# Kernel optimization log

Measured on AMD Instinct MI355X. Metric: run time of the kernel, lower is better.

## Reference

```python
import jax, jax.numpy as jnp
import numpy as np

UNITS = [100, 80, 50, 30]
D_IN = 64


def _lstm_layer(x, Wx, Wh, b):
    # x: [B, T, D]; Wx: [D, 4u]; Wh: [u, 4u]; b: [4u]
    B = x.shape[0]
    u = Wh.shape[0]
    # precompute input contribution for all timesteps: [B, T, 4u]
    xg = jnp.einsum('btd,dg->btg', x, Wx) + b

    def step(carry, xg_t):
        h, c = carry
        g = xg_t + h @ Wh                      # [B, 4u]
        i, f, cbar, o = jnp.split(g, 4, axis=-1)
        i = jax.nn.sigmoid(i)
        f = jax.nn.sigmoid(f)
        o = jax.nn.sigmoid(o)
        c = f * c + i * jnp.tanh(cbar)
        h = o * jnp.tanh(c)
        return (h, c), h

    init = (jnp.zeros((B, u), x.dtype), jnp.zeros((B, u), x.dtype))
    (h_final, _), hs = jax.lax.scan(step, init, jnp.swapaxes(xg, 0, 1))
    return jnp.swapaxes(hs, 0, 1), h_final  # [B, T, u], [B, u]


def setup_inputs() -> dict:
    key = jax.random.key(0)
    ks = jax.random.split(key, 16)
    B, T = 256, 1024
    inp = {"sequence": jax.random.normal(ks[0], (B, T, D_IN), dtype=jnp.float32)}
    d_in = D_IN
    for li, u in enumerate(UNITS):
        s_x = 1.0 / np.sqrt(d_in)
        s_h = 1.0 / np.sqrt(u)
        inp[f"Wx{li}"] = jax.random.normal(ks[1 + 3 * li], (d_in, 4 * u), dtype=jnp.float32) * s_x
        inp[f"Wh{li}"] = jax.random.normal(ks[2 + 3 * li], (u, 4 * u), dtype=jnp.float32) * s_h
        inp[f"b{li}"] = jnp.zeros((4 * u,), dtype=jnp.float32)
        d_in = u
    inp["W_out"] = jax.random.normal(ks[13], (UNITS[-1], 1), dtype=jnp.float32) / np.sqrt(UNITS[-1])
    inp["b_out"] = jnp.zeros((1,), dtype=jnp.float32)
    return inp


def reference(sequence, Wx0, Wh0, b0, Wx1, Wh1, b1, Wx2, Wh2, b2, Wx3, Wh3, b3, W_out, b_out):
    # 4 stacked LSTM layers; dropout is identity at inference.
    x, _ = _lstm_layer(sequence, Wx0, Wh0, b0)   # [B, T, 100]
    x, _ = _lstm_layer(x, Wx1, Wh1, b1)          # [B, T, 80]
    x, _ = _lstm_layer(x, Wx2, Wh2, b2)          # [B, T, 50]
    _, h = _lstm_layer(x, Wx3, Wh3, b3)          # final state [B, 30]
    return h @ W_out + b_out                     # [B, 1]
```

## Files before the change

### kernel.cpp

```cpp
#include <hip/hip_runtime.h>


#define BATCH 256
#define TFULL 1024
#define TC    128
#define NCHUNK (TFULL / TC)

__device__ __forceinline__ float fast_rcp(float x) {
    return __builtin_amdgcn_rcpf(x);
}

__device__ __forceinline__ float tanh_fast(float x) {
    float e = __expf(-2.0f * fabsf(x));
    float r = fast_rcp(1.0f + e);
    return copysignf(fmaf(2.0f, r, -1.0f), x);
}

__device__ __forceinline__ void lds_barrier() {
    asm volatile("s_waitcnt lgkmcnt(0)\n\ts_barrier" ::: "memory");
}

template<int CTRL>
__device__ __forceinline__ float dpp_add(float v) {
    int t = __builtin_amdgcn_update_dpp(0, __float_as_int(v), CTRL, 0xF, 0xF, true);
    return v + __int_as_float(t);
}
template<int CTRL>
__device__ __forceinline__ float dpp_mov(float v) {
    int t = __builtin_amdgcn_update_dpp(0, __float_as_int(v), CTRL, 0xF, 0xF, true);
    return __int_as_float(t);
}

template<int K, int N>
__global__ __launch_bounds__(256, 2)
void xg_gemm(const float* __restrict__ x, int batchStride,
             const float* __restrict__ Wx,
             const float* __restrict__ bias,
             float* __restrict__ out)
{
    constexpr int K4   = (K + 3) / 4;
    constexpr int SLAB = 64 * 4 + 4;

    const int n0   = blockIdx.x * 64;
    const int row0 = blockIdx.y * 64;
    const int tid  = threadIdx.x;
    const int tx   = tid & 15;
    const int ty   = tid >> 4;

    __shared__ __align__(16) float s_A[K4 * SLAB];
    __shared__ __align__(16) float s_B[K4 * 4 * 64];

    if constexpr ((K % 4) == 0) {
        for (int i = tid; i < 64 * (K / 4); i += 256) {
            const int row = i / (K / 4);
            const int k4  = i % (K / 4);
            const int gr  = row0 + row;
            const int b   = gr >> 7;
            const int t   = gr & 127;
            float4 v = *(const float4*)(x + (size_t)b * batchStride + t * K + k4 * 4);
            *(float4*)(s_A + k4 * SLAB + row * 4) = v;
        }
    } else {
        for (int i = tid; i < 64 * K; i += 256) {
            const int row = i / K;
            const int k   = i % K;
            const int gr  = row0 + row;
            const int b   = gr >> 7;
            const int t   = gr & 127;
            s_A[(k >> 2) * SLAB + row * 4 + (k & 3)] =
                x[(size_t)b * batchStride + t * K + k];
        }
        constexpr int PAD = K4 * 4 - K;
        for (int i = tid; i < 64 * PAD; i += 256) {
            const int row = i / PAD;
            const int kk  = K + i % PAD;
            s_A[(kk >> 2) * SLAB + row * 4 + (kk & 3)] = 0.0f;
        }
    }

    for (int i = tid; i < K4 * 4 * 16; i += 256) {
        const int k  = i >> 4;
        const int c4 = i & 15;
        float4 v = {0.0f, 0.0f, 0.0f, 0.0f};
        if (k < K && n0 + c4 * 4 < N)
            v = *(const float4*)(Wx + (size_t)k * N + n0 + c4 * 4);
        *(float4*)(s_B + k * 64 + c4 * 4) = v;
    }
    __syncthreads();

    float acc[4][4];
#pragma unroll
    for (int r = 0; r < 4; ++r)
#pragma unroll
        for (int c = 0; c < 4; ++c) acc[r][c] = 0.0f;

    for (int k4 = 0; k4 < K4; ++k4) {
        float4 bv[4];
#pragma unroll
        for (int j = 0; j < 4; ++j)
            bv[j] = *(const float4*)(s_B + (k4 * 4 + j) * 64 + tx * 4);
#pragma unroll
        for (int r = 0; r < 4; ++r) {
            float4 av = *(const float4*)(s_A + k4 * SLAB + (ty + 16 * r) * 4);
#pragma unroll
            for (int c = 0; c < 4; ++c) {
                acc[r][c] = fmaf(av.x, ((const float*)&bv[0])[c], acc[r][c]);
                acc[r][c] = fmaf(av.y, ((const float*)&bv[1])[c], acc[r][c]);
                acc[r][c] = fmaf(av.z, ((const float*)&bv[2])[c], acc[r][c]);
                acc[r][c] = fmaf(av.w, ((const float*)&bv[3])[c], acc[r][c]);
            }
        }
    }

    if (n0 + tx * 4 < N) {
        float4 bb = *(const float4*)(bias + n0 + tx * 4);
#pragma unroll
        for (int r = 0; r < 4; ++r) {
            float4 o;
            o.x = acc[r][0] + bb.x;
            o.y = acc[r][1] + bb.y;
            o.z = acc[r][2] + bb.z;
            o.w = acc[r][3] + bb.w;
            *(float4*)(out + (size_t)(row0 + ty + 16 * r) * N + n0 + tx * 4) = o;
        }
    }
}

template<int U, int S, int BLOCK, bool LAST>
__device__ __forceinline__ void rec_body(
    const float* __restrict__ xg,
    const float* __restrict__ Wh,
    float* __restrict__ xout,
    float* __restrict__ c_state,
    float* __restrict__ h_state,
    int first,
    const float* __restrict__ Wout,
    const float* __restrict__ bout,
    float* __restrict__ dout)
{
    constexpr int G = 4 * U;

    const int b   = blockIdx.x;
    const int tid = threadIdx.x;
    const int u   = tid >> 2;
    const int s   = tid & 3;
    const bool act_th = (u < U);
    const int uu  = act_th ? u : 0;

    __shared__ __align__(16) float s_h[2][4 * S];

    float w4[4][S];
#pragma unroll
    for (int g = 0; g < 4; ++g)
#pragma unroll
        for (int kk = 0; kk < S; ++kk) {
            const int k = s * S + kk;
            w4[g][kk] = (act_th && k < U) ? Wh[(size_t)k * G + g * U + uu] : 0.0f;
        }

    for (int i = tid; i < 2 * 4 * S; i += BLOCK) ((float*)s_h)[i] = 0.0f;
    __syncthreads();
    if (tid < U) s_h[0][tid] = first ? 0.0f : h_state[b * U + tid];
    float c = first ? 0.0f : c_state[b * U + uu];
    __syncthreads();

    const float* xgp = xg + (size_t)b * TC * G + (s * U + uu);
    float xg0 = xgp[0];
    float xg1 = xgp[G];

    int cur = 0;
    float h = 0.0f, hprev = 0.0f;
    const bool is_t = (s == 2);

    for (int t = 0; t < TC; ++t, cur ^= 1) {
        const int tp = (t + 2 < TC) ? (t + 2) : (TC - 1);
        const float xg2 = xgp[(size_t)tp * G];

        if (!LAST) {
            if (act_th && s == 0 && t > 0)
                xout[((size_t)b * TC + (t - 1)) * U + u] = hprev;
        }

        float a0 = 0.0f, a1 = 0.0f, a2 = 0.0f, a3 = 0.0f;
        const float* hs = &s_h[cur][s * S];
#pragma unroll
        for (int kk = 0; kk < S; kk += 4) {
            float4 v = *(const float4*)(hs + kk);
            a0 = fmaf(v.x, w4[0][kk + 0], a0);
            a0 = fmaf(v.y, w4[0][kk + 1], a0);
            a0 = fmaf(v.z, w4[0][kk + 2], a0);
            a0 = fmaf(v.w, w4[0][kk + 3], a0);
            a1 = fmaf(v.x, w4[1][kk + 0], a1);
            a1 = fmaf(v.y, w4[1][kk + 1], a1);
            a1 = fmaf(v.z, w4[1][kk + 2], a1);
            a1 = fmaf(v.w, w4[1][kk + 3], a1);
            a2 = fmaf(v.x, w4[2][kk + 0], a2);
            a2 = fmaf(v.y, w4[2][kk + 1], a2);
            a2 = fmaf(v.z, w4[2][kk + 2], a2);
            a2 = fmaf(v.w, w4[2][kk + 3], a2);
            a3 = fmaf(v.x, w4[3][kk + 0], a3);
            a3 = fmaf(v.y, w4[3][kk + 1], a3);
            a3 = fmaf(v.z, w4[3][kk + 2], a3);
            a3 = fmaf(v.w, w4[3][kk + 3], a3);
        }

        a0 = dpp_add<0xB1>(a0); a0 = dpp_add<0x4E>(a0);
        a1 = dpp_add<0xB1>(a1); a1 = dpp_add<0x4E>(a1);
        a2 = dpp_add<0xB1>(a2); a2 = dpp_add<0x4E>(a2);
        a3 = dpp_add<0xB1>(a3); a3 = dpp_add<0x4E>(a3);

        const float asum = (s == 0) ? a0 : (s == 1) ? a1 : (s == 2) ? a2 : a3;
        const float gs = asum + xg0;
        const float y  = is_t ? (-2.0f * fabsf(gs)) : (-gs);
        const float r  = fast_rcp(1.0f + __expf(y));
        const float v  = is_t ? copysignf(fmaf(2.0f, r, -1.0f), gs) : r;

        const float fi = dpp_mov<0x00>(v);
        const float ff = dpp_mov<0x55>(v);
        const float tc = dpp_mov<0xAA>(v);
        const float fo = dpp_mov<0xFF>(v);
        c = fmaf(ff, c, fi * tc);
        h = fo * tanh_fast(c);

        const int nxt = cur ^ 1;
        if (act_th && s == 0) s_h[nxt][u] = h;
        hprev = h;
        xg0 = xg1; xg1 = xg2;
        lds_barrier();
    }

    if (!LAST) {
        if (act_th && s == 0)
            xout[((size_t)b * TC + (TC - 1)) * U + u] = hprev;
    }
    if (act_th && s == 0) {
        c_state[b * U + u] = c;
        h_state[b * U + u] = h;
    }
    if (LAST && tid == 0) {
        float acc = bout[0];
#pragma unroll
        for (int k = 0; k < U; ++k) acc = fmaf(s_h[cur][k], Wout[k], acc);
        dout[b] = acc;
    }
}

#define REC_ARGS const float* __restrict__ xg, const float* __restrict__ Wh,        \
                 float* __restrict__ xout, float* __restrict__ c_state,             \
                 float* __restrict__ h_state, int first,                            \
                 const float* __restrict__ Wout, const float* __restrict__ bout,    \
                 float* __restrict__ dout
#define REC_PASS xg, Wh, xout, c_state, h_state, first, Wout, bout, dout

__attribute__((amdgpu_flat_work_group_size(448, 448), amdgpu_waves_per_eu(1, 2)))
__global__ void rec_l0(REC_ARGS) { rec_body<100, 28, 448, false>(REC_PASS); }

__attribute__((amdgpu_flat_work_group_size(320, 320), amdgpu_waves_per_eu(1, 2)))
__global__ void rec_l1(REC_ARGS) { rec_body<80, 20, 320, false>(REC_PASS); }

__attribute__((amdgpu_flat_work_group_size(256, 256), amdgpu_waves_per_eu(1, 2)))
__global__ void rec_l2(REC_ARGS) { rec_body<50, 16, 256, false>(REC_PASS); }

__attribute__((amdgpu_flat_work_group_size(128, 128), amdgpu_waves_per_eu(1, 2)))
__global__ void rec_l3(REC_ARGS) { rec_body<30, 8, 128, true>(REC_PASS); }

extern "C" void kernel_launch(void* const* d_in, const int* in_sizes, int n_in,
                              void* d_out, int out_size, void* d_ws, size_t ws_size,
                              hipStream_t stream)
{
    const float* seq  = (const float*)d_in[0];
    const float* Wx0  = (const float*)d_in[1];
    const float* Wh0  = (const float*)d_in[2];
    const float* b0   = (const float*)d_in[3];
    const float* Wx1  = (const float*)d_in[4];
    const float* Wh1  = (const float*)d_in[5];
    const float* b1   = (const float*)d_in[6];
    const float* Wx2  = (const float*)d_in[7];
    const float* Wh2  = (const float*)d_in[8];
    const float* b2   = (const float*)d_in[9];
    const float* Wx3  = (const float*)d_in[10];
    const float* Wh3  = (const float*)d_in[11];
    const float* b3   = (const float*)d_in[12];
    const float* Wout = (const float*)d_in[13];
    const float* bout = (const float*)d_in[14];
    float* out = (float*)d_out;

    const size_t XG_ELEMS = (size_t)BATCH * TC * 400;
    const size_t XC_ELEMS = (size_t)BATCH * TC * 100;
    float* ws  = (float*)d_ws;
    float* XGa = ws;
    float* XGb = XGa + XG_ELEMS;
    float* Xca = XGb + XG_ELEMS;
    float* Xcb = Xca + XC_ELEMS;
    float* st  = Xcb + XC_ELEMS;
    float* c0 = st + 0 * 32768; float* h0 = st + 1 * 32768;
    float* c1 = st + 2 * 32768; float* h1 = st + 3 * 32768;
    float* c2 = st + 4 * 32768; float* h2 = st + 5 * 32768;
    float* c3 = st + 6 * 32768; float* h3 = st + 7 * 32768;

    const dim3 gB(BATCH);

    for (int j = 0; j < NCHUNK; ++j) {
        const int first = (j == 0) ? 1 : 0;

        xg_gemm<64, 400><<<dim3(7, 512), 256, 0, stream>>>(
            seq + (size_t)j * TC * 64, TFULL * 64, Wx0, b0, XGa);
        rec_l0<<<gB, 448, 0, stream>>>(
            XGa, Wh0, Xca, c0, h0, first, nullptr, nullptr, nullptr);

        xg_gemm<100, 320><<<dim3(5, 512), 256, 0, stream>>>(
            Xca, TC * 100, Wx1, b1, XGb);
        rec_l1<<<gB, 320, 0, stream>>>(
            XGb, Wh1, Xcb, c1, h1, first, nullptr, nullptr, nullptr);

        xg_gemm<80, 200><<<dim3(4, 512), 256, 0, stream>>>(
            Xcb, TC * 80, Wx2, b2, XGa);
        rec_l2<<<gB, 256, 0, stream>>>(
            XGa, Wh2, Xca, c2, h2, first, nullptr, nullptr, nullptr);

        xg_gemm<50, 120><<<dim3(2, 512), 256, 0, stream>>>(
            Xca, TC * 50, Wx3, b3, XGb);
        rec_l3<<<gB, 128, 0, stream>>>(
            XGb, Wh3, nullptr, c3, h3, first, Wout, bout, out);
    }
}
```

Baseline: 2.912 ms.

## Wavefront-pipeline the four LSTM layers across time chunks in merged launches

Replaces the layer-by-layer loop with a diagonal wavefront schedule. At each diagonal step, one merged GEMM launch computes input projections for all active layers, and one merged recurrent launch runs all four layers on different time chunks at once. The chunk size drops from 128 to 64, which gives more diagonal steps but shorter serial chains per launch. The goal is to fill the GPU with 1024 concurrent blocks instead of 256 and to cut the number of launches. The cost is that the smaller layers run 448-thread blocks with idle waves, and per-layer workspace buffers are now needed.

```diff
diff --git a/kernel.cpp b/kernel.cpp
--- a/kernel.cpp
+++ b/kernel.cpp
@@ -3,8 +3,9 @@
 
 #define BATCH 256
 #define TFULL 1024
-#define TC    128
+#define TC    64
 #define NCHUNK (TFULL / TC)
+#define NDIAG  (NCHUNK + 3)
 
 __device__ __forceinline__ float fast_rcp(float x) {
     return __builtin_amdgcn_rcpf(x);
@@ -32,31 +33,33 @@
 }
 
 template<int K, int N>
-__global__ __launch_bounds__(256, 2)
-void xg_gemm(const float* __restrict__ x, int batchStride,
-             const float* __restrict__ Wx,
-             const float* __restrict__ bias,
-             float* __restrict__ out)
+__device__ __forceinline__ void gemm_body(
+    const float* __restrict__ x, int batchStride,
+    const float* __restrict__ Wx,
+    const float* __restrict__ bias,
+    float* __restrict__ out,
+    int lid, float* __restrict__ smem)
 {
     constexpr int K4   = (K + 3) / 4;
     constexpr int SLAB = 64 * 4 + 4;
-
-    const int n0   = blockIdx.x * 64;
-    const int row0 = blockIdx.y * 64;
+    constexpr int GX   = (N + 63) / 64;
+
+    float* s_A = smem;
+    float* s_B = smem + K4 * SLAB;
+
+    const int n0   = (lid % GX) * 64;
+    const int row0 = (lid / GX) * 64;
     const int tid  = threadIdx.x;
     const int tx   = tid & 15;
     const int ty   = tid >> 4;
-
-    __shared__ __align__(16) float s_A[K4 * SLAB];
-    __shared__ __align__(16) float s_B[K4 * 4 * 64];
 
     if constexpr ((K % 4) == 0) {
         for (int i = tid; i < 64 * (K / 4); i += 256) {
             const int row = i / (K / 4);
             const int k4  = i % (K / 4);
             const int gr  = row0 + row;
-            const int b   = gr >> 7;
-            const int t   = gr & 127;
+            const int b   = gr >> 6;
+            const int t   = gr & 63;
             float4 v = *(const float4*)(x + (size_t)b * batchStride + t * K + k4 * 4);
             *(float4*)(s_A + k4 * SLAB + row * 4) = v;
         }
@@ -65,8 +68,8 @@
             const int row = i / K;
             const int k   = i % K;
             const int gr  = row0 + row;
-            const int b   = gr >> 7;
-            const int t   = gr & 127;
+            const int b   = gr >> 6;
+            const int t   = gr & 63;
             s_A[(k >> 2) * SLAB + row * 4 + (k & 3)] =
                 x[(size_t)b * batchStride + t * K + k];
         }
@@ -126,28 +129,50 @@
     }
 }
 
+struct GemmArgs {
+    const float *x0, *x1, *x2, *x3;
+    float *o0, *o1, *o2, *o3;
+    const float *Wx0, *bi0, *Wx1, *bi1, *Wx2, *bi2, *Wx3, *bi3;
+    int off1, off2, off3;
+};
+
+__global__ __launch_bounds__(256, 2)
+void xg_all(GemmArgs a)
+{
+    __shared__ __align__(16) float smem[12900];
+    const int bid = blockIdx.x;
+    if (bid < a.off1)
+        gemm_body<64, 400>(a.x0, TFULL * 64, a.Wx0, a.bi0, a.o0, bid, smem);
+    else if (bid < a.off2)
+        gemm_body<100, 320>(a.x1, TC * 100, a.Wx1, a.bi1, a.o1, bid - a.off1, smem);
+    else if (bid < a.off3)
+        gemm_body<80, 200>(a.x2, TC * 80, a.Wx2, a.bi2, a.o2, bid - a.off2, smem);
+    else
+        gemm_body<50, 120>(a.x3, TC * 50, a.Wx3, a.bi3, a.o3, bid - a.off3, smem);
+}
+
 template<int U, int S, int BLOCK, bool LAST>
-__device__ __forceinline__ void rec_body(
+__device__ __forceinline__ void rec4_body(
+    float* __restrict__ s_h,
     const float* __restrict__ xg,
     const float* __restrict__ Wh,
     float* __restrict__ xout,
     float* __restrict__ c_state,
     float* __restrict__ h_state,
-    int first,
+    int first, int b,
     const float* __restrict__ Wout,
     const float* __restrict__ bout,
     float* __restrict__ dout)
 {
-    constexpr int G = 4 * U;
-
-    const int b   = blockIdx.x;
+    constexpr int G  = 4 * U;
+    constexpr int HS = 4 * S;
+
     const int tid = threadIdx.x;
     const int u   = tid >> 2;
     const int s   = tid & 3;
     const bool act_th = (u < U);
     const int uu  = act_th ? u : 0;
-
-    __shared__ __align__(16) float s_h[2][4 * S];
+    const bool wave_act = ((tid & ~63) < 4 * U);
 
     float w4[4][S];
 #pragma unroll
@@ -158,9 +183,9 @@
             w4[g][kk] = (act_th && k < U) ? Wh[(size_t)k * G + g * U + uu] : 0.0f;
         }
 
-    for (int i = tid; i < 2 * 4 * S; i += BLOCK) ((float*)s_h)[i] = 0.0f;
+    for (int i = tid; i < 2 * HS; i += BLOCK) s_h[i] = 0.0f;
     __syncthreads();
-    if (tid < U) s_h[0][tid] = first ? 0.0f : h_state[b * U + tid];
+    if (tid < U) s_h[tid] = first ? 0.0f : h_state[b * U + tid];
     float c = first ? 0.0f : c_state[b * U + uu];
     __syncthreads();
 
@@ -173,59 +198,61 @@
     const bool is_t = (s == 2);
 
     for (int t = 0; t < TC; ++t, cur ^= 1) {
-        const int tp = (t + 2 < TC) ? (t + 2) : (TC - 1);
-        const float xg2 = xgp[(size_t)tp * G];
-
-        if (!LAST) {
-            if (act_th && s == 0 && t > 0)
-                xout[((size_t)b * TC + (t - 1)) * U + u] = hprev;
-        }
-
-        float a0 = 0.0f, a1 = 0.0f, a2 = 0.0f, a3 = 0.0f;
-        const float* hs = &s_h[cur][s * S];
-#pragma unroll
-        for (int kk = 0; kk < S; kk += 4) {
-            float4 v = *(const float4*)(hs + kk);
-            a0 = fmaf(v.x, w4[0][kk + 0], a0);
-            a0 = fmaf(v.y, w4[0][kk + 1], a0);
-            a0 = fmaf(v.z, w4[0][kk + 2], a0);
-            a0 = fmaf(v.w, w4[0][kk + 3], a0);
-            a1 = fmaf(v.x, w4[1][kk + 0], a1);
-            a1 = fmaf(v.y, w4[1][kk + 1], a1);
-            a1 = fmaf(v.z, w4[1][kk + 2], a1);
-            a1 = fmaf(v.w, w4[1][kk + 3], a1);
-            a2 = fmaf(v.x, w4[2][kk + 0], a2);
-            a2 = fmaf(v.y, w4[2][kk + 1], a2);
-            a2 = fmaf(v.z, w4[2][kk + 2], a2);
-            a2 = fmaf(v.w, w4[2][kk + 3], a2);
-            a3 = fmaf(v.x, w4[3][kk + 0], a3);
-            a3 = fmaf(v.y, w4[3][kk + 1], a3);
-            a3 = fmaf(v.z, w4[3][kk + 2], a3);
-            a3 = fmaf(v.w, w4[3][kk + 3], a3);
-        }
-
-        a0 = dpp_add<0xB1>(a0); a0 = dpp_add<0x4E>(a0);
-        a1 = dpp_add<0xB1>(a1); a1 = dpp_add<0x4E>(a1);
-        a2 = dpp_add<0xB1>(a2); a2 = dpp_add<0x4E>(a2);
-        a3 = dpp_add<0xB1>(a3); a3 = dpp_add<0x4E>(a3);
-
-        const float asum = (s == 0) ? a0 : (s == 1) ? a1 : (s == 2) ? a2 : a3;
-        const float gs = asum + xg0;
-        const float y  = is_t ? (-2.0f * fabsf(gs)) : (-gs);
-        const float r  = fast_rcp(1.0f + __expf(y));
-        const float v  = is_t ? copysignf(fmaf(2.0f, r, -1.0f), gs) : r;
-
-        const float fi = dpp_mov<0x00>(v);
-        const float ff = dpp_mov<0x55>(v);
-        const float tc = dpp_mov<0xAA>(v);
-        const float fo = dpp_mov<0xFF>(v);
-        c = fmaf(ff, c, fi * tc);
-        h = fo * tanh_fast(c);
-
-        const int nxt = cur ^ 1;
-        if (act_th && s == 0) s_h[nxt][u] = h;
-        hprev = h;
-        xg0 = xg1; xg1 = xg2;
+        if (wave_act) {
+            const int tp = (t + 2 < TC) ? (t + 2) : (TC - 1);
+            const float xg2 = xgp[(size_t)tp * G];
+
+            if (!LAST) {
+                if (act_th && s == 0 && t > 0)
+                    xout[((size_t)b * TC + (t - 1)) * U + u] = hprev;
+            }
+
+            float a0 = 0.0f, a1 = 0.0f, a2 = 0.0f, a3 = 0.0f;
+            const float* hs = s_h + cur * HS + s * S;
+#pragma unroll
+            for (int kk = 0; kk < S; kk += 4) {
+                float4 v = *(const float4*)(hs + kk);
+                a0 = fmaf(v.x, w4[0][kk + 0], a0);
+                a0 = fmaf(v.y, w4[0][kk + 1], a0);
+                a0 = fmaf(v.z, w4[0][kk + 2], a0);
+                a0 = fmaf(v.w, w4[0][kk + 3], a0);
+                a1 = fmaf(v.x, w4[1][kk + 0], a1);
+                a1 = fmaf(v.y, w4[1][kk + 1], a1);
+                a1 = fmaf(v.z, w4[1][kk + 2], a1);
+                a1 = fmaf(v.w, w4[1][kk + 3], a1);
+                a2 = fmaf(v.x, w4[2][kk + 0], a2);
+                a2 = fmaf(v.y, w4[2][kk + 1], a2);
+                a2 = fmaf(v.z, w4[2][kk + 2], a2);
+                a2 = fmaf(v.w, w4[2][kk + 3], a2);
+                a3 = fmaf(v.x, w4[3][kk + 0], a3);
+                a3 = fmaf(v.y, w4[3][kk + 1], a3);
+                a3 = fmaf(v.z, w4[3][kk + 2], a3);
+                a3 = fmaf(v.w, w4[3][kk + 3], a3);
+            }
+
+            a0 = dpp_add<0xB1>(a0); a0 = dpp_add<0x4E>(a0);
+            a1 = dpp_add<0xB1>(a1); a1 = dpp_add<0x4E>(a1);
+            a2 = dpp_add<0xB1>(a2); a2 = dpp_add<0x4E>(a2);
+            a3 = dpp_add<0xB1>(a3); a3 = dpp_add<0x4E>(a3);
+
+            const float asum = (s == 0) ? a0 : (s == 1) ? a1 : (s == 2) ? a2 : a3;
+            const float gs = asum + xg0;
+            const float y  = is_t ? (-2.0f * fabsf(gs)) : (-gs);
+            const float r  = fast_rcp(1.0f + __expf(y));
+            const float v  = is_t ? copysignf(fmaf(2.0f, r, -1.0f), gs) : r;
+
+            const float fi = dpp_mov<0x00>(v);
+            const float ff = dpp_mov<0x55>(v);
+            const float tc = dpp_mov<0xAA>(v);
+            const float fo = dpp_mov<0xFF>(v);
+            c = fmaf(ff, c, fi * tc);
+            h = fo * tanh_fast(c);
+
+            const int nxt = cur ^ 1;
+            if (act_th && s == 0) s_h[nxt * HS + u] = h;
+            hprev = h;
+            xg0 = xg1; xg1 = xg2;
+        }
         lds_barrier();
     }
 
@@ -240,29 +267,42 @@
     if (LAST && tid == 0) {
         float acc = bout[0];
 #pragma unroll
-        for (int k = 0; k < U; ++k) acc = fmaf(s_h[cur][k], Wout[k], acc);
+        for (int k = 0; k < U; ++k) acc = fmaf(s_h[cur * HS + k], Wout[k], acc);
         dout[b] = acc;
     }
 }
 
-#define REC_ARGS const float* __restrict__ xg, const float* __restrict__ Wh,        \
-                 float* __restrict__ xout, float* __restrict__ c_state,             \
-                 float* __restrict__ h_state, int first,                            \
-                 const float* __restrict__ Wout, const float* __restrict__ bout,    \
-                 float* __restrict__ dout
-#define REC_PASS xg, Wh, xout, c_state, h_state, first, Wout, bout, dout
-
-__attribute__((amdgpu_flat_work_group_size(448, 448), amdgpu_waves_per_eu(1, 2)))
-__global__ void rec_l0(REC_ARGS) { rec_body<100, 28, 448, false>(REC_PASS); }
-
-__attribute__((amdgpu_flat_work_group_size(320, 320), amdgpu_waves_per_eu(1, 2)))
-__global__ void rec_l1(REC_ARGS) { rec_body<80, 20, 320, false>(REC_PASS); }
-
-__attribute__((amdgpu_flat_work_group_size(256, 256), amdgpu_waves_per_eu(1, 2)))
-__global__ void rec_l2(REC_ARGS) { rec_body<50, 16, 256, false>(REC_PASS); }
-
-__attribute__((amdgpu_flat_work_group_size(128, 128), amdgpu_waves_per_eu(1, 2)))
-__global__ void rec_l3(REC_ARGS) { rec_body<30, 8, 128, true>(REC_PASS); }
+struct RecArgs {
+    const float *xg0, *xg1, *xg2, *xg3;
+    const float *Wh0, *Wh1, *Wh2, *Wh3;
+    float *xc0, *xc1, *xc2;
+    float *c0, *h0, *c1, *h1, *c2, *h2, *c3, *h3;
+    const float *Wout, *bout;
+    float *dout;
+    int d;
+};
+
+__global__ __attribute__((amdgpu_flat_work_group_size(448, 448),
+                          amdgpu_waves_per_eu(4, 8)))
+void rec_all(RecArgs a)
+{
+    __shared__ __align__(16) float s_h[2 * 112];
+    const int grp = blockIdx.x >> 8;
+    const int b   = blockIdx.x & 255;
+    const int j   = a.d - grp;
+    if (j < 0 || j >= NCHUNK) return;
+    const int first = (j == 0) ? 1 : 0;
+    switch (grp) {
+    case 0: rec4_body<100, 28, 448, false>(s_h, a.xg0, a.Wh0, a.xc0, a.c0, a.h0,
+                                           first, b, nullptr, nullptr, nullptr); break;
+    case 1: rec4_body< 80, 20, 448, false>(s_h, a.xg1, a.Wh1, a.xc1, a.c1, a.h1,
+                                           first, b, nullptr, nullptr, nullptr); break;
+    case 2: rec4_body< 50, 16, 448, false>(s_h, a.xg2, a.Wh2, a.xc2, a.c2, a.h2,
+                                           first, b, nullptr, nullptr, nullptr); break;
+    default: rec4_body< 30,  8, 448, true >(s_h, a.xg3, a.Wh3, nullptr, a.c3, a.h3,
+                                           first, b, a.Wout, a.bout, a.dout); break;
+    }
+}
 
 extern "C" void kernel_launch(void* const* d_in, const int* in_sizes, int n_in,
                               void* d_out, int out_size, void* d_ws, size_t ws_size,
@@ -285,42 +325,48 @@
     const float* bout = (const float*)d_in[14];
     float* out = (float*)d_out;
 
-    const size_t XG_ELEMS = (size_t)BATCH * TC * 400;
-    const size_t XC_ELEMS = (size_t)BATCH * TC * 100;
     float* ws  = (float*)d_ws;
-    float* XGa = ws;
-    float* XGb = XGa + XG_ELEMS;
-    float* Xca = XGb + XG_ELEMS;
-    float* Xcb = Xca + XC_ELEMS;
-    float* st  = Xcb + XC_ELEMS;
-    float* c0 = st + 0 * 32768; float* h0 = st + 1 * 32768;
-    float* c1 = st + 2 * 32768; float* h1 = st + 3 * 32768;
-    float* c2 = st + 4 * 32768; float* h2 = st + 5 * 32768;
-    float* c3 = st + 6 * 32768; float* h3 = st + 7 * 32768;
-
-    const dim3 gB(BATCH);
-
-    for (int j = 0; j < NCHUNK; ++j) {
-        const int first = (j == 0) ? 1 : 0;
-
-        xg_gemm<64, 400><<<dim3(7, 512), 256, 0, stream>>>(
-            seq + (size_t)j * TC * 64, TFULL * 64, Wx0, b0, XGa);
-        rec_l0<<<gB, 448, 0, stream>>>(
-            XGa, Wh0, Xca, c0, h0, first, nullptr, nullptr, nullptr);
-
-        xg_gemm<100, 320><<<dim3(5, 512), 256, 0, stream>>>(
-            Xca, TC * 100, Wx1, b1, XGb);
-        rec_l1<<<gB, 320, 0, stream>>>(
-            XGb, Wh1, Xcb, c1, h1, first, nullptr, nullptr, nullptr);
-
-        xg_gemm<80, 200><<<dim3(4, 512), 256, 0, stream>>>(
-            Xcb, TC * 80, Wx2, b2, XGa);
-        rec_l2<<<gB, 256, 0, stream>>>(
-            XGa, Wh2, Xca, c2, h2, first, nullptr, nullptr, nullptr);
-
-        xg_gemm<50, 120><<<dim3(2, 512), 256, 0, stream>>>(
-            Xca, TC * 50, Wx3, b3, XGb);
-        rec_l3<<<gB, 128, 0, stream>>>(
-            XGb, Wh3, nullptr, c3, h3, first, Wout, bout, out);
-    }
-}
+    float* XG0 = ws;
+    float* XG1 = XG0 + (size_t)BATCH * TC * 400;
+    float* XG2 = XG1 + (size_t)BATCH * TC * 320;
+    float* XG3 = XG2 + (size_t)BATCH * TC * 200;
+    float* XC0 = XG3 + (size_t)BATCH * TC * 120;
+    float* XC1 = XC0 + (size_t)BATCH * TC * 100;
+    float* XC2 = XC1 + (size_t)BATCH * TC * 80;
+    float* st  = XC2 + (size_t)BATCH * TC * 50;
+    float* sc0 = st + 0 * 32768; float* sh0 = st + 1 * 32768;
+    float* sc1 = st + 2 * 32768; float* sh1 = st + 3 * 32768;
+    float* sc2 = st + 4 * 32768; float* sh2 = st + 5 * 32768;
+    float* sc3 = st + 6 * 32768; float* sh3 = st + 7 * 32768;
+
+    const int NB0 = 7 * 256, NB1 = 5 * 256, NB2 = 4 * 256, NB3 = 2 * 256;
+
+    for (int d = 0; d < NDIAG; ++d) {
+        GemmArgs ga;
+        ga.x0 = nullptr; ga.x1 = nullptr; ga.x2 = nullptr; ga.x3 = nullptr;
+        ga.o0 = XG0; ga.o1 = XG1; ga.o2 = XG2; ga.o3 = XG3;
+        ga.Wx0 = Wx0; ga.bi0 = b0; ga.Wx1 = Wx1; ga.bi1 = b1;
+        ga.Wx2 = Wx2; ga.bi2 = b2; ga.Wx3 = Wx3; ga.bi3 = b3;
+        int nb = 0;
+        if (d < NCHUNK)                { ga.x0 = seq + (size_t)d * TC * 64; nb += NB0; }
+        ga.off1 = nb;
+        if (d >= 1 && d - 1 < NCHUNK)  { ga.x1 = XC0; nb += NB1; }
+        ga.off2 = nb;
+        if (d >= 2 && d - 2 < NCHUNK)  { ga.x2 = XC1; nb += NB2; }
+        ga.off3 = nb;
+        if (d >= 3 && d - 3 < NCHUNK)  { ga.x3 = XC2; nb += NB3; }
+
+        xg_all<<<dim3(nb), dim3(256), 0, stream>>>(ga);
+
+        RecArgs ra;
+        ra.xg0 = XG0; ra.xg1 = XG1; ra.xg2 = XG2; ra.xg3 = XG3;
+        ra.Wh0 = Wh0; ra.Wh1 = Wh1; ra.Wh2 = Wh2; ra.Wh3 = Wh3;
+        ra.xc0 = XC0; ra.xc1 = XC1; ra.xc2 = XC2;
+        ra.c0 = sc0; ra.h0 = sh0; ra.c1 = sc1; ra.h1 = sh1;
+        ra.c2 = sc2; ra.h2 = sh2; ra.c3 = sc3; ra.h3 = sh3;
+        ra.Wout = Wout; ra.bout = bout; ra.dout = out;
+        ra.d = d;
+
+        rec_all<<<dim3(4 * 256), dim3(448), 0, stream>>>(ra);
+    }
+}
```

Measured after the change: 2.880 ms. No clear change (-1.1%).

## Use fp16 dot2 recurrent matvec with 8 lanes per hidden unit

Applied to the files above, without the earlier changes.

Each recurrent kernel now stores hidden state and recurrent weights in fp16 and computes the h·Wh matvec with v_dot2_f32_f16. Work per hidden unit is split across 8 lanes instead of 4, so the block size doubles and the per-lane reduction chain is shorter; the DPP reduction gains one extra step. Whole waves with no active units skip the step body. The goal is a shorter serial per-timestep latency, at the cost of fp16 rounding of h and Wh, more threads per block, and one more reduction stage.

```diff
diff --git a/kernel.cpp b/kernel.cpp
--- a/kernel.cpp
+++ b/kernel.cpp
@@ -6,6 +6,9 @@
 #define TC    128
 #define NCHUNK (TFULL / TC)
 
+typedef __attribute__((ext_vector_type(2))) _Float16 f16x2;
+typedef __attribute__((ext_vector_type(4))) _Float16 f16x4;
+
 __device__ __forceinline__ float fast_rcp(float x) {
     return __builtin_amdgcn_rcpf(x);
 }
@@ -14,6 +17,16 @@
     float e = __expf(-2.0f * fabsf(x));
     float r = fast_rcp(1.0f + e);
     return copysignf(fmaf(2.0f, r, -1.0f), x);
+}
+
+__device__ __forceinline__ float fdot2_(f16x2 a, f16x2 b, float c) {
+#if __has_builtin(__builtin_amdgcn_fdot2)
+    return __builtin_amdgcn_fdot2(a, b, c, false);
+#else
+    float d;
+    asm("v_dot2_f32_f16 %0, %1, %2, %3" : "=v"(d) : "v"(a), "v"(b), "v"(c));
+    return d;
+#endif
 }
 
 __device__ __forceinline__ void lds_barrier() {
@@ -127,7 +140,8 @@
 }
 
 template<int U, int S, int BLOCK, bool LAST>
-__device__ __forceinline__ void rec_body(
+__device__ __forceinline__ void rec8_body(
+    _Float16* __restrict__ s_h,
     const float* __restrict__ xg,
     const float* __restrict__ Wh,
     float* __restrict__ xout,
@@ -138,94 +152,95 @@
     const float* __restrict__ bout,
     float* __restrict__ dout)
 {
-    constexpr int G = 4 * U;
+    constexpr int G  = 4 * U;
+    constexpr int HS = 8 * S;
 
     const int b   = blockIdx.x;
     const int tid = threadIdx.x;
-    const int u   = tid >> 2;
-    const int s   = tid & 3;
+    const int u   = tid >> 3;
+    const int s   = tid & 7;
+    const int g   = s & 3;
     const bool act_th = (u < U);
     const int uu  = act_th ? u : 0;
-
-    __shared__ __align__(16) float s_h[2][4 * S];
-
-    float w4[4][S];
-#pragma unroll
-    for (int g = 0; g < 4; ++g)
-#pragma unroll
-        for (int kk = 0; kk < S; ++kk) {
-            const int k = s * S + kk;
-            w4[g][kk] = (act_th && k < U) ? Wh[(size_t)k * G + g * U + uu] : 0.0f;
-        }
-
-    for (int i = tid; i < 2 * 4 * S; i += BLOCK) ((float*)s_h)[i] = 0.0f;
+    const bool wave_act = ((tid & ~63) < 8 * U);
+
+    f16x2 w[4][S / 2];
+#pragma unroll
+    for (int gg = 0; gg < 4; ++gg)
+#pragma unroll
+        for (int p = 0; p < S / 2; ++p) {
+            const int k0 = s * S + 2 * p;
+            const int k1 = k0 + 1;
+            const float wa = (act_th && k0 < U) ? Wh[(size_t)k0 * G + gg * U + uu] : 0.0f;
+            const float wb = (act_th && k1 < U) ? Wh[(size_t)k1 * G + gg * U + uu] : 0.0f;
+            w[gg][p] = (f16x2){(_Float16)wa, (_Float16)wb};
+        }
+
+    for (int i = tid; i < 2 * HS; i += BLOCK) s_h[i] = (_Float16)0.0f;
     __syncthreads();
-    if (tid < U) s_h[0][tid] = first ? 0.0f : h_state[b * U + tid];
+    if (tid < U) s_h[tid] = (_Float16)(first ? 0.0f : h_state[b * U + tid]);
     float c = first ? 0.0f : c_state[b * U + uu];
     __syncthreads();
 
-    const float* xgp = xg + (size_t)b * TC * G + (s * U + uu);
+    const float* xgp = xg + (size_t)b * TC * G + (g * U + uu);
     float xg0 = xgp[0];
     float xg1 = xgp[G];
 
     int cur = 0;
     float h = 0.0f, hprev = 0.0f;
-    const bool is_t = (s == 2);
+    const bool is_t = (g == 2);
 
     for (int t = 0; t < TC; ++t, cur ^= 1) {
-        const int tp = (t + 2 < TC) ? (t + 2) : (TC - 1);
-        const float xg2 = xgp[(size_t)tp * G];
-
-        if (!LAST) {
-            if (act_th && s == 0 && t > 0)
-                xout[((size_t)b * TC + (t - 1)) * U + u] = hprev;
-        }
-
-        float a0 = 0.0f, a1 = 0.0f, a2 = 0.0f, a3 = 0.0f;
-        const float* hs = &s_h[cur][s * S];
-#pragma unroll
-        for (int kk = 0; kk < S; kk += 4) {
-            float4 v = *(const float4*)(hs + kk);
-            a0 = fmaf(v.x, w4[0][kk + 0], a0);
-            a0 = fmaf(v.y, w4[0][kk + 1], a0);
-            a0 = fmaf(v.z, w4[0][kk + 2], a0);
-            a0 = fmaf(v.w, w4[0][kk + 3], a0);
-            a1 = fmaf(v.x, w4[1][kk + 0], a1);
-            a1 = fmaf(v.y, w4[1][kk + 1], a1);
-            a1 = fmaf(v.z, w4[1][kk + 2], a1);
-            a1 = fmaf(v.w, w4[1][kk + 3], a1);
-            a2 = fmaf(v.x, w4[2][kk + 0], a2);
-            a2 = fmaf(v.y, w4[2][kk + 1], a2);
-            a2 = fmaf(v.z, w4[2][kk + 2], a2);
-            a2 = fmaf(v.w, w4[2][kk + 3], a2);
-            a3 = fmaf(v.x, w4[3][kk + 0], a3);
-            a3 = fmaf(v.y, w4[3][kk + 1], a3);
-            a3 = fmaf(v.z, w4[3][kk + 2], a3);
-            a3 = fmaf(v.w, w4[3][kk + 3], a3);
-        }
-
-        a0 = dpp_add<0xB1>(a0); a0 = dpp_add<0x4E>(a0);
-        a1 = dpp_add<0xB1>(a1); a1 = dpp_add<0x4E>(a1);
-        a2 = dpp_add<0xB1>(a2); a2 = dpp_add<0x4E>(a2);
-        a3 = dpp_add<0xB1>(a3); a3 = dpp_add<0x4E>(a3);
-
-        const float asum = (s == 0) ? a0 : (s == 1) ? a1 : (s == 2) ? a2 : a3;
-        const float gs = asum + xg0;
-        const float y  = is_t ? (-2.0f * fabsf(gs)) : (-gs);
-        const float r  = fast_rcp(1.0f + __expf(y));
-        const float v  = is_t ? copysignf(fmaf(2.0f, r, -1.0f), gs) : r;
-
-        const float fi = dpp_mov<0x00>(v);
-        const float ff = dpp_mov<0x55>(v);
-        const float tc = dpp_mov<0xAA>(v);
-        const float fo = dpp_mov<0xFF>(v);
-        c = fmaf(ff, c, fi * tc);
-        h = fo * tanh_fast(c);
-
-        const int nxt = cur ^ 1;
-        if (act_th && s == 0) s_h[nxt][u] = h;
-        hprev = h;
-        xg0 = xg1; xg1 = xg2;
+        if (wave_act) {
+            const int tp = (t + 2 < TC) ? (t + 2) : (TC - 1);
+            const float xg2 = xgp[(size_t)tp * G];
+
+            if (!LAST) {
+                if (act_th && s == 0 && t > 0)
+                    xout[((size_t)b * TC + (t - 1)) * U + u] = hprev;
+            }
+
+            float a0 = 0.0f, a1 = 0.0f, a2 = 0.0f, a3 = 0.0f;
+            const _Float16* hs = s_h + cur * HS + s * S;
+#pragma unroll
+            for (int kk = 0; kk < S; kk += 4) {
+                f16x4 v = *(const f16x4*)(hs + kk);
+                f16x2 lo = __builtin_shufflevector(v, v, 0, 1);
+                f16x2 hi = __builtin_shufflevector(v, v, 2, 3);
+                const int p = kk >> 1;
+                a0 = fdot2_(lo, w[0][p],     a0);
+                a0 = fdot2_(hi, w[0][p + 1], a0);
+                a1 = fdot2_(lo, w[1][p],     a1);
+                a1 = fdot2_(hi, w[1][p + 1], a1);
+                a2 = fdot2_(lo, w[2][p],     a2);
+                a2 = fdot2_(hi, w[2][p + 1], a2);
+                a3 = fdot2_(lo, w[3][p],     a3);
+                a3 = fdot2_(hi, w[3][p + 1], a3);
+            }
+
+            a0 = dpp_add<0xB1>(a0); a0 = dpp_add<0x4E>(a0); a0 = dpp_add<0x141>(a0);
+            a1 = dpp_add<0xB1>(a1); a1 = dpp_add<0x4E>(a1); a1 = dpp_add<0x141>(a1);
+            a2 = dpp_add<0xB1>(a2); a2 = dpp_add<0x4E>(a2); a2 = dpp_add<0x141>(a2);
+            a3 = dpp_add<0xB1>(a3); a3 = dpp_add<0x4E>(a3); a3 = dpp_add<0x141>(a3);
+
+            const float asum = (g == 0) ? a0 : (g == 1) ? a1 : (g == 2) ? a2 : a3;
+            const float gs = asum + xg0;
+            const float y  = is_t ? (-2.0f * fabsf(gs)) : (-gs);
+            const float r  = fast_rcp(1.0f + __expf(y));
+            const float v  = is_t ? copysignf(fmaf(2.0f, r, -1.0f), gs) : r;
+
+            const float fi = dpp_mov<0x00>(v);
+            const float ff = dpp_mov<0x55>(v);
+            const float tc = dpp_mov<0xAA>(v);
+            const float fo = dpp_mov<0xFF>(v);
+            c = fmaf(ff, c, fi * tc);
+            h = fo * tanh_fast(c);
+
+            const int nxt = cur ^ 1;
+            if (act_th && s == 0) s_h[nxt * HS + u] = (_Float16)h;
+            hprev = h;
+            xg0 = xg1; xg1 = xg2;
+        }
         lds_barrier();
     }
 
@@ -240,7 +255,8 @@
     if (LAST && tid == 0) {
         float acc = bout[0];
 #pragma unroll
-        for (int k = 0; k < U; ++k) acc = fmaf(s_h[cur][k], Wout[k], acc);
+        for (int k = 0; k < U; ++k)
+            acc = fmaf((float)s_h[cur * HS + k], Wout[k], acc);
         dout[b] = acc;
     }
 }
@@ -252,17 +268,29 @@
                  float* __restrict__ dout
 #define REC_PASS xg, Wh, xout, c_state, h_state, first, Wout, bout, dout
 
-__attribute__((amdgpu_flat_work_group_size(448, 448), amdgpu_waves_per_eu(1, 2)))
-__global__ void rec_l0(REC_ARGS) { rec_body<100, 28, 448, false>(REC_PASS); }
-
-__attribute__((amdgpu_flat_work_group_size(320, 320), amdgpu_waves_per_eu(1, 2)))
-__global__ void rec_l1(REC_ARGS) { rec_body<80, 20, 320, false>(REC_PASS); }
-
-__attribute__((amdgpu_flat_work_group_size(256, 256), amdgpu_waves_per_eu(1, 2)))
-__global__ void rec_l2(REC_ARGS) { rec_body<50, 16, 256, false>(REC_PASS); }
-
-__attribute__((amdgpu_flat_work_group_size(128, 128), amdgpu_waves_per_eu(1, 2)))
-__global__ void rec_l3(REC_ARGS) { rec_body<30, 8, 128, true>(REC_PASS); }
+__attribute__((amdgpu_flat_work_group_size(832, 832), amdgpu_waves_per_eu(4, 8)))
+__global__ void rec_l0(REC_ARGS) {
+    __shared__ __align__(16) _Float16 s_h[2 * 8 * 16];
+    rec8_body<100, 16, 832, false>(s_h, REC_PASS);
+}
+
+__attribute__((amdgpu_flat_work_group_size(640, 640), amdgpu_waves_per_eu(4, 8)))
+__global__ void rec_l1(REC_ARGS) {
+    __shared__ __align__(16) _Float16 s_h[2 * 8 * 12];
+    rec8_body<80, 12, 640, false>(s_h, REC_PASS);
+}
+
+__attribute__((amdgpu_flat_work_group_size(448, 448), amdgpu_waves_per_eu(4, 8)))
+__global__ void rec_l2(REC_ARGS) {
+    __shared__ __align__(16) _Float16 s_h[2 * 8 * 8];
+    rec8_body<50, 8, 448, false>(s_h, REC_PASS);
+}
+
+__attribute__((amdgpu_flat_work_group_size(256, 256), amdgpu_waves_per_eu(4, 8)))
+__global__ void rec_l3(REC_ARGS) {
+    __shared__ __align__(16) _Float16 s_h[2 * 8 * 4];
+    rec8_body<30, 4, 256, true>(s_h, REC_PASS);
+}
 
 extern "C" void kernel_launch(void* const* d_in, const int* in_sizes, int n_in,
                               void* d_out, int out_size, void* d_ws, size_t ws_size,
@@ -305,22 +333,22 @@
 
         xg_gemm<64, 400><<<dim3(7, 512), 256, 0, stream>>>(
             seq + (size_t)j * TC * 64, TFULL * 64, Wx0, b0, XGa);
-        rec_l0<<<gB, 448, 0, stream>>>(
+        rec_l0<<<gB, 832, 0, stream>>>(
             XGa, Wh0, Xca, c0, h0, first, nullptr, nullptr, nullptr);
 
         xg_gemm<100, 320><<<dim3(5, 512), 256, 0, stream>>>(
             Xca, TC * 100, Wx1, b1, XGb);
-        rec_l1<<<gB, 320, 0, stream>>>(
+        rec_l1<<<gB, 640, 0, stream>>>(
             XGb, Wh1, Xcb, c1, h1, first, nullptr, nullptr, nullptr);
 
         xg_gemm<80, 200><<<dim3(4, 512), 256, 0, stream>>>(
             Xcb, TC * 80, Wx2, b2, XGa);
-        rec_l2<<<gB, 256, 0, stream>>>(
+        rec_l2<<<gB, 448, 0, stream>>>(
             XGa, Wh2, Xca, c2, h2, first, nullptr, nullptr, nullptr);
 
         xg_gemm<50, 120><<<dim3(2, 512), 256, 0, stream>>>(
             Xca, TC * 50, Wx3, b3, XGb);
-        rec_l3<<<gB, 128, 0, stream>>>(
+        rec_l3<<<gB, 256, 0, stream>>>(
             XGb, Wh3, nullptr, c3, h3, first, Wout, bout, out);
     }
 }
```

Result: slower. 3.608 ms (+23.9%).
